# Performance work log

Measured on AMD Instinct MI355X. Metric: run time of the kernel, lower is better.

## Reference

```python
import jax, jax.numpy as jnp
import numpy as np

D_STATE = 8
DT_RANK = 8  # ceil(128/16)


def _grouped_1x1(x, w):
    # x: (B,H,W,Cin), w: (g, Cout//g, Cin//g)
    B, H, W, _ = x.shape
    g, o, i = w.shape
    xg = x.reshape(B, H, W, g, i)
    return jnp.einsum('bhwgi,goi->bhwgo', xg, w).reshape(B, H, W, g * o)


def setup_inputs() -> dict:
    key = jax.random.key(0)
    ks = jax.random.split(key, 16)
    B, H, W, C = 8, 64, 64, 128
    g = 4
    D = 128  # expand_dim = d_inner
    N = D_STATE
    R = DT_RANK
    inp = {}
    inp['x'] = jax.random.normal(ks[0], (B, H, W, C), dtype=jnp.float32)
    inp['w1'] = jax.random.normal(ks[1], (g, D // g, C // g), dtype=jnp.float32) * 0.1
    inp['dw'] = jax.random.normal(ks[2], (3, 3, 1, D), dtype=jnp.float32) * 0.1  # HWIO depthwise
    inp['in_proj_w'] = jax.random.normal(ks[3], (2 * D, D), dtype=jnp.float32) * 0.05
    inp['conv1d_w'] = jax.random.normal(ks[4], (D, 3), dtype=jnp.float32) * 0.1
    inp['conv1d_b'] = jax.random.normal(ks[5], (D,), dtype=jnp.float32) * 0.05
    inp['x_proj_w'] = jax.random.normal(ks[6], (R + 2 * N, D), dtype=jnp.float32) * 0.05
    inp['dt_proj_w'] = jax.random.normal(ks[7], (D, R), dtype=jnp.float32) * 0.05
    inp['dt_proj_b'] = jax.random.normal(ks[8], (D,), dtype=jnp.float32) * 0.05
    inp['A_log'] = jnp.log(jnp.tile(jnp.arange(1, N + 1, dtype=jnp.float32)[None, :], (D, 1)))
    inp['D_param'] = jnp.ones((D,), dtype=jnp.float32)
    inp['out_proj_w'] = jax.random.normal(ks[9], (D, D), dtype=jnp.float32) * 0.05
    inp['gamma'] = jnp.ones((D,), dtype=jnp.float32)
    inp['beta'] = jnp.zeros((D,), dtype=jnp.float32)
    inp['w2'] = jax.random.normal(ks[10], (g, D // g, C // g), dtype=jnp.float32) * 0.1
    inp['wout'] = jax.random.normal(ks[11], (g, C // g, D // g), dtype=jnp.float32) * 0.1
    return inp


def _mamba(x_seq, in_proj_w, conv1d_w, conv1d_b, x_proj_w, dt_proj_w, dt_proj_b, A_log, D_param, out_proj_w):
    # x_seq: (B, L, D)
    B, L, D = x_seq.shape
    N, R = D_STATE, DT_RANK
    xz = jnp.einsum('bld,ed->ble', x_seq, in_proj_w)  # (B,L,2D)
    u, z = xz[..., :D], xz[..., D:]
    # causal depthwise conv1d, kernel=3, left pad 2 (torch: padding=2, slice [:L])
    up = jnp.pad(u, ((0, 0), (2, 0), (0, 0)))
    u = (up[:, 0:L] * conv1d_w[:, 0] + up[:, 1:L + 1] * conv1d_w[:, 1]
         + up[:, 2:L + 2] * conv1d_w[:, 2] + conv1d_b)
    u = jax.nn.silu(u)
    x_dbl = jnp.einsum('bld,ed->ble', u, x_proj_w)  # (B,L,R+2N)
    dt = x_dbl[..., :R]
    Bm = x_dbl[..., R:R + N]
    Cm = x_dbl[..., R + N:]
    delta = jax.nn.softplus(jnp.einsum('blr,dr->bld', dt, dt_proj_w) + dt_proj_b)  # (B,L,D)
    A = -jnp.exp(A_log)  # (D,N)

    def step(h, inp):
        d_t, u_t, b_t, c_t = inp  # (B,D),(B,D),(B,N),(B,N)
        dA = jnp.exp(d_t[..., None] * A)            # (B,D,N)
        h = dA * h + (d_t * u_t)[..., None] * b_t[:, None, :]
        y_t = jnp.einsum('bdn,bn->bd', h, c_t)
        return h, y_t

    h0 = jnp.zeros((B, D, N), dtype=x_seq.dtype)
    xs = (jnp.swapaxes(delta, 0, 1), jnp.swapaxes(u, 0, 1),
          jnp.swapaxes(Bm, 0, 1), jnp.swapaxes(Cm, 0, 1))
    _, ys = jax.lax.scan(step, h0, xs)              # ys: (L,B,D)
    y = jnp.swapaxes(ys, 0, 1) + u * D_param
    y = y * jax.nn.silu(z)
    return jnp.einsum('bld,ed->ble', y, out_proj_w)


def reference(x, w1, dw, in_proj_w, conv1d_w, conv1d_b, x_proj_w, dt_proj_w, dt_proj_b,
              A_log, D_param, out_proj_w, gamma, beta, w2, wout):
    B, H, W, C = x.shape
    D = dw.shape[-1]
    x1 = _grouped_1x1(x, w1)  # (B,H,W,D)
    x1 = jax.lax.conv_general_dilated(
        x1, dw, window_strides=(1, 1), padding='SAME',
        feature_group_count=D, dimension_numbers=('NHWC', 'HWIO', 'NHWC'))
    x1 = jax.nn.silu(x1)
    x1_seq = x1.reshape(B, H * W, D)
    x1_seq = _mamba(x1_seq, in_proj_w, conv1d_w, conv1d_b, x_proj_w,
                    dt_proj_w, dt_proj_b, A_log, D_param, out_proj_w)
    x1 = x1_seq.reshape(B, H, W, D)
    mu = jnp.mean(x1, axis=-1, keepdims=True)
    var = jnp.mean(jnp.square(x1 - mu), axis=-1, keepdims=True)
    x1 = (x1 - mu) * jax.lax.rsqrt(var + 1e-5) * gamma + beta
    x2 = jax.nn.silu(_grouped_1x1(x, w2))
    x_fuse = x1 * x2
    return _grouped_1x1(x_fuse, wout)  # (B,H,W,C)
```

## Files before the change

kernel.cpp:

```cpp
#include <hip/hip_runtime.h>
#include <math.h>

#define B_    8
#define C_    128
#define D_    128
#define L_    4096
#define NPOS_ 32768
#define NC_   256
#define S_    16
#define MFL_  1048576

typedef __attribute__((ext_vector_type(8))) short short8;
typedef __attribute__((ext_vector_type(4))) float f32x4;

__device__ __forceinline__ float siluf(float x) { return x / (1.f + __expf(-x)); }
__device__ __forceinline__ float softplusf(float x) {
    if (x > 20.f) return x;
    return __logf(1.f + __expf(x));
}
__device__ __forceinline__ unsigned short f2bf(float f) {
    unsigned int u = __float_as_uint(f);
    u = (u + 0x7FFFu + ((u >> 16) & 1u)) >> 16;
    return (unsigned short)u;
}
__device__ __forceinline__ float bf2f(unsigned short h) {
    return __uint_as_float(((unsigned int)h) << 16);
}
__device__ __forceinline__ void scan_as(float dl, const float* Ar, bool fast, float* a) {
    if (fast) {
        float e1 = __expf(-dl);
        a[0] = e1;
        a[1] = e1 * e1;
        a[2] = a[1] * e1;
        a[3] = a[1] * a[1];
        a[4] = a[3] * e1;
        a[5] = a[3] * a[1];
        a[6] = a[5] * e1;
        a[7] = a[3] * a[3];
    } else {
        #pragma unroll
        for (int n = 0; n < 8; ++n) a[n] = __expf(dl * Ar[n]);
    }
}

__global__ __launch_bounds__(256) void k1_g1x1(const float* __restrict__ x,
                                               const float* __restrict__ w1,
                                               const float* __restrict__ w2,
                                               const float* __restrict__ inW,
                                               const float* __restrict__ OW,
                                               const float* __restrict__ xpw,
                                               unsigned short* __restrict__ inWb,
                                               unsigned short* __restrict__ OWb,
                                               unsigned short* __restrict__ xpwb,
                                               unsigned short* __restrict__ t1b,
                                               unsigned short* __restrict__ x2sb) {
    __shared__ float xs[16 * 128];
    int t = threadIdx.x;
    {
        int i = blockIdx.x * 51 + t;
        if (t < 51 && i < 52224) {
            if (i < 32768)      inWb[i] = f2bf(inW[i]);
            else if (i < 49152) OWb[i - 32768] = f2bf(OW[i - 32768]);
            else                xpwb[i - 49152] = f2bf(xpw[i - 49152]);
        }
    }
    int d = t & 127, ph = t >> 7;
    int g = d >> 5, o = d & 31;
    float w1r[32], w2r[32];
    #pragma unroll
    for (int i = 0; i < 32; ++i) {
        w1r[i] = w1[g * 1024 + o * 32 + i];
        w2r[i] = w2[g * 1024 + o * 32 + i];
    }
    int pos0 = blockIdx.x * 32;
    for (int it = 0; it < 2; ++it) {
        int p0 = pos0 + it * 16;
        #pragma unroll
        for (int q = 0; q < 2; ++q) {
            int fi = t * 2 + q;
            *(float4*)&xs[fi * 4] = *(const float4*)&x[p0 * 128 + fi * 4];
        }
        __syncthreads();
        #pragma unroll
        for (int q = 0; q < 8; ++q) {
            int pl = ph * 8 + q;
            float a1 = 0.f, a2 = 0.f;
            const float* xr = &xs[pl * 128 + g * 32];
            #pragma unroll
            for (int i4 = 0; i4 < 8; ++i4) {
                float4 xv = *(const float4*)&xr[i4 * 4];
                a1 += xv.x * w1r[i4*4] + xv.y * w1r[i4*4+1] + xv.z * w1r[i4*4+2] + xv.w * w1r[i4*4+3];
                a2 += xv.x * w2r[i4*4] + xv.y * w2r[i4*4+1] + xv.z * w2r[i4*4+2] + xv.w * w2r[i4*4+3];
            }
            int pos = p0 + pl;
            t1b[pos * 128 + d]  = f2bf(a1);
            x2sb[pos * 128 + d] = f2bf(siluf(a2));
        }
        __syncthreads();
    }
}

__global__ __launch_bounds__(128) void k2_dwconv(const unsigned short* __restrict__ t1b,
                                                 const float* __restrict__ dw,
                                                 unsigned short* __restrict__ x1cb) {
    int d = threadIdx.x;
    float dwr[9];
    #pragma unroll
    for (int k = 0; k < 9; ++k) dwr[k] = dw[k * 128 + d];
    int bid = blockIdx.x;
    int wt = bid & 15, ht = (bid >> 4) & 7, b = bid >> 7;
    int h0 = ht * 8, w0 = wt * 4;
    float rows[10][6];
    #pragma unroll
    for (int r = 0; r < 10; ++r) {
        int hh = h0 - 1 + r;
        bool hv = (hh >= 0) && (hh < 64);
        #pragma unroll
        for (int c = 0; c < 6; ++c) {
            int w = w0 - 1 + c;
            bool wvv = (w >= 0) && (w < 64);
            rows[r][c] = (hv && wvv) ? bf2f(t1b[((b * 64 + hh) * 64 + w) * 128 + d]) : 0.f;
        }
    }
    #pragma unroll
    for (int hi = 0; hi < 8; ++hi) {
        #pragma unroll
        for (int wi = 0; wi < 4; ++wi) {
            float acc = rows[hi][wi]     * dwr[0] + rows[hi][wi+1]   * dwr[1] + rows[hi][wi+2]   * dwr[2]
                      + rows[hi+1][wi]   * dwr[3] + rows[hi+1][wi+1] * dwr[4] + rows[hi+1][wi+2] * dwr[5]
                      + rows[hi+2][wi]   * dwr[6] + rows[hi+2][wi+1] * dwr[7] + rows[hi+2][wi+2] * dwr[8];
            x1cb[((b * 64 + h0 + hi) * 64 + w0 + wi) * 128 + d] = f2bf(siluf(acc));
        }
    }
}

__global__ __launch_bounds__(256) void k3_mfma(const unsigned short* __restrict__ Abf,
                                               const unsigned short* __restrict__ Bbf,
                                               unsigned short* __restrict__ urawb,
                                               unsigned short* __restrict__ zb) {
    __shared__ unsigned short Al[64 * 72];
    __shared__ unsigned short Bl[128 * 72];
    int t = threadIdx.x;
    int pos0 = (blockIdx.x >> 1) * 64;
    int half = blockIdx.x & 1;
    const unsigned short* Bh = Bbf + (size_t)half * 128 * 128;
    unsigned short* dst = half ? zb : urawb;
    int lane = t & 63, wv = t >> 6;
    int lanem = lane & 15, laneq = lane >> 4;
    f32x4 acc[8];
    #pragma unroll
    for (int i = 0; i < 8; ++i) acc[i] = (f32x4){0.f, 0.f, 0.f, 0.f};
    for (int kc = 0; kc < 2; ++kc) {
        #pragma unroll
        for (int q = 0; q < 2; ++q) {
            int c = t + q * 256;
            int row = c >> 3, col = c & 7;
            *(int4*)&Al[row * 72 + col * 8] = *(const int4*)&Abf[(pos0 + row) * 128 + kc * 64 + col * 8];
        }
        #pragma unroll
        for (int q = 0; q < 4; ++q) {
            int c = t + q * 256;
            int row = c >> 3, col = c & 7;
            *(int4*)&Bl[row * 72 + col * 8] = *(const int4*)&Bh[row * 128 + kc * 64 + col * 8];
        }
        __syncthreads();
        #pragma unroll
        for (int ks = 0; ks < 2; ++ks) {
            short8 af = *(const short8*)&Al[(wv * 16 + lanem) * 72 + ks * 32 + laneq * 8];
            #pragma unroll
            for (int ni = 0; ni < 8; ++ni) {
                short8 bfr = *(const short8*)&Bl[(ni * 16 + lanem) * 72 + ks * 32 + laneq * 8];
                acc[ni] = __builtin_amdgcn_mfma_f32_16x16x32_bf16(af, bfr, acc[ni], 0, 0, 0);
            }
        }
        __syncthreads();
    }
    #pragma unroll
    for (int ni = 0; ni < 8; ++ni)
        #pragma unroll
        for (int r = 0; r < 4; ++r) {
            int m = pos0 + wv * 16 + laneq * 4 + r;
            int n = ni * 16 + lanem;
            dst[m * 128 + n] = f2bf(acc[ni][r]);
        }
}

__global__ __launch_bounds__(256) void k45_convproj(const unsigned short* __restrict__ urawb,
                                                    const float* __restrict__ cw,
                                                    const float* __restrict__ cb,
                                                    const unsigned short* __restrict__ xpwb,
                                                    const float* __restrict__ dtw,
                                                    const float* __restrict__ dtb,
                                                    const float* __restrict__ A_log,
                                                    unsigned short* __restrict__ usb,
                                                    unsigned short* __restrict__ deltab,
                                                    float* __restrict__ Bm,
                                                    float* __restrict__ Cm,
                                                    float* __restrict__ cA,
                                                    float* __restrict__ cB) {
    __shared__ unsigned short uA[32 * 136];
    __shared__ unsigned short xB[32 * 136];
    __shared__ float xdb[32 * 36];
    int t = threadIdx.x;
    int d = t & 127, ph = t >> 7;
    for (int i = t; i < 32 * 128; i += 256) {
        int n = i >> 7, k = i & 127;
        xB[n * 136 + k] = (n < 24) ? xpwb[n * 128 + k] : (unsigned short)0;
    }
    float cw0 = cw[d * 3 + 0], cw1 = cw[d * 3 + 1], cw2 = cw[d * 3 + 2], cbr = cb[d];
    float dtwr[8];
    #pragma unroll
    for (int r = 0; r < 8; ++r) dtwr[r] = dtw[d * 8 + r];
    float dtbr = dtb[d];
    float Ar[8]; bool fast = true;
    #pragma unroll
    for (int n = 0; n < 8; ++n) {
        Ar[n] = -__expf(A_log[d * 8 + n]);
        fast = fast && (fabsf(Ar[n] + (float)(n + 1)) < 2e-3f);
    }

    int gpos0 = blockIdx.x * 32;
    int ll0 = (gpos0 & 4095) + ph * 16;
    int base = (gpos0 + ph * 16) * 128 + d;
    float ur0 = (ll0 >= 2) ? bf2f(urawb[base - 256]) : 0.f;
    float ur1 = (ll0 >= 1) ? bf2f(urawb[base - 128]) : 0.f;
    #pragma unroll
    for (int q = 0; q < 16; ++q) {
        float urq = bf2f(urawb[base + q * 128]);
        float v = siluf(ur0 * cw0 + ur1 * cw1 + urq * cw2 + cbr);
        unsigned short vb = f2bf(v);
        usb[base + q * 128] = vb;
        uA[(ph * 16 + q) * 136 + d] = vb;
        ur0 = ur1; ur1 = urq;
    }
    __syncthreads();
    int lane = t & 63, wv = t >> 6;
    int lanem = lane & 15, laneq = lane >> 4;
    int m0 = (wv & 1) * 16, n0 = (wv >> 1) * 16;
    f32x4 accx = (f32x4){0.f, 0.f, 0.f, 0.f};
    #pragma unroll
    for (int ks = 0; ks < 4; ++ks) {
        short8 af  = *(const short8*)&uA[(m0 + lanem) * 136 + ks * 32 + laneq * 8];
        short8 bfr = *(const short8*)&xB[(n0 + lanem) * 136 + ks * 32 + laneq * 8];
        accx = __builtin_amdgcn_mfma_f32_16x16x32_bf16(af, bfr, accx, 0, 0, 0);
    }
    #pragma unroll
    for (int r = 0; r < 4; ++r)
        xdb[(m0 + laneq * 4 + r) * 36 + n0 + lanem] = accx[r];
    __syncthreads();
    float h[8], ap[8];
    #pragma unroll
    for (int n = 0; n < 8; ++n) { h[n] = 0.f; ap[n] = 1.f; }
    #pragma unroll
    for (int q = 0; q < 16; ++q) {
        int pl = ph * 16 + q;
        float dt = dtbr;
        #pragma unroll
        for (int r = 0; r < 8; ++r) dt += xdb[pl * 36 + r] * dtwr[r];
        unsigned short dlb = f2bf(softplusf(dt));
        deltab[base + q * 128] = dlb;
        float dl = bf2f(dlb);
        float du = dl * bf2f(uA[pl * 136 + d]);
        float a[8];
        scan_as(dl, Ar, fast, a);
        #pragma unroll
        for (int n = 0; n < 8; ++n) {
            ap[n] *= a[n];
            h[n] = a[n] * h[n] + du * xdb[pl * 36 + 8 + n];
        }
    }
    int bH = gpos0 >> 12;
    int c  = ((gpos0 & 4095) >> 4) + ph;
    int obase = ((bH * NC_ + c) * 128 + d) * 8;
    *(float4*)&cA[obase]     = make_float4(ap[0], ap[1], ap[2], ap[3]);
    *(float4*)&cA[obase + 4] = make_float4(ap[4], ap[5], ap[6], ap[7]);
    *(float4*)&cB[obase]     = make_float4(h[0], h[1], h[2], h[3]);
    *(float4*)&cB[obase + 4] = make_float4(h[4], h[5], h[6], h[7]);
    for (int i = t; i < 512; i += 256) {
        int p = i >> 4, j = i & 15;
        float v = xdb[p * 36 + 8 + j];
        int gp = gpos0 + p;
        if (j < 8) Bm[gp * 8 + j] = v;
        else       Cm[gp * 8 + (j - 8)] = v;
    }
}

__global__ __launch_bounds__(128) void k6_scan2(const float* __restrict__ cA,
                                                const float* __restrict__ cB,
                                                float* __restrict__ carry) {
    int b = blockIdx.x >> 3;
    int slice = blockIdx.x & 7;
    int dn = slice * 128 + threadIdx.x;
    float h = 0.f;
    #pragma unroll 8
    for (int c = 0; c < NC_; ++c) {
        int idx = (b * NC_ + c) * 1024 + dn;
        float a  = cA[idx];
        float bv = cB[idx];
        carry[idx] = h;
        h = a * h + bv;
    }
}

__global__ __launch_bounds__(128) void k7_scan3(const unsigned short* __restrict__ deltab,
                                                const unsigned short* __restrict__ usb,
                                                const float* __restrict__ Bm,
                                                const float* __restrict__ Cm,
                                                const unsigned short* __restrict__ zb,
                                                const float* __restrict__ A_log,
                                                const float* __restrict__ Dp,
                                                const float* __restrict__ carry,
                                                unsigned short* __restrict__ ybf) {
    int d = threadIdx.x;
    int bc = blockIdx.x;
    int b = bc >> 8, c = bc & 255;
    float Ar[8]; bool fast = true;
    #pragma unroll
    for (int n = 0; n < 8; ++n) {
        Ar[n] = -__expf(A_log[d * 8 + n]);
        fast = fast && (fabsf(Ar[n] + (float)(n + 1)) < 2e-3f);
    }
    float Dpr = Dp[d];
    int cbase = ((b * NC_ + c) * 128 + d) * 8;
    float4 h0 = *(const float4*)&carry[cbase];
    float4 h1 = *(const float4*)&carry[cbase + 4];
    float h[8] = {h0.x, h0.y, h0.z, h0.w, h1.x, h1.y, h1.z, h1.w};
    int base  = (b * L_ + c * S_) * 128 + d;
    int bbase = (b * L_ + c * S_) * 8;
    #pragma unroll
    for (int s = 0; s < S_; ++s) {
        float dl = bf2f(deltab[base + s * 128]);
        float uv = bf2f(usb[base + s * 128]);
        float zv = bf2f(zb[base + s * 128]);
        float du = dl * uv;
        float4 bm0 = *(const float4*)&Bm[bbase + s * 8];
        float4 bm1 = *(const float4*)&Bm[bbase + s * 8 + 4];
        float4 cm0 = *(const float4*)&Cm[bbase + s * 8];
        float4 cm1 = *(const float4*)&Cm[bbase + s * 8 + 4];
        float a[8];
        scan_as(dl, Ar, fast, a);
        h[0] = a[0] * h[0] + du * bm0.x;
        h[1] = a[1] * h[1] + du * bm0.y;
        h[2] = a[2] * h[2] + du * bm0.z;
        h[3] = a[3] * h[3] + du * bm0.w;
        h[4] = a[4] * h[4] + du * bm1.x;
        h[5] = a[5] * h[5] + du * bm1.y;
        h[6] = a[6] * h[6] + du * bm1.z;
        h[7] = a[7] * h[7] + du * bm1.w;
        float yv = h[0] * cm0.x + h[1] * cm0.y + h[2] * cm0.z + h[3] * cm0.w
                 + h[4] * cm1.x + h[5] * cm1.y + h[6] * cm1.z + h[7] * cm1.w;
        yv = (yv + uv * Dpr) * siluf(zv);
        ybf[base + s * 128] = f2bf(yv);
    }
}

__global__ __launch_bounds__(256) void k8a_mfma(const unsigned short* __restrict__ Abf,
                                                const unsigned short* __restrict__ Bbf,
                                                unsigned short* __restrict__ xzb) {
    __shared__ unsigned short Al[64 * 72];
    __shared__ unsigned short Bl[128 * 72];
    int t = threadIdx.x;
    int pos0 = blockIdx.x * 64;
    int lane = t & 63, wv = t >> 6;
    int lanem = lane & 15, laneq = lane >> 4;
    f32x4 acc[8];
    #pragma unroll
    for (int i = 0; i < 8; ++i) acc[i] = (f32x4){0.f, 0.f, 0.f, 0.f};
    for (int kc = 0; kc < 2; ++kc) {
        #pragma unroll
        for (int q = 0; q < 2; ++q) {
            int c = t + q * 256;
            int row = c >> 3, col = c & 7;
            *(int4*)&Al[row * 72 + col * 8] = *(const int4*)&Abf[(pos0 + row) * 128 + kc * 64 + col * 8];
        }
        #pragma unroll
        for (int q = 0; q < 4; ++q) {
            int c = t + q * 256;
            int row = c >> 3, col = c & 7;
            *(int4*)&Bl[row * 72 + col * 8] = *(const int4*)&Bbf[row * 128 + kc * 64 + col * 8];
        }
        __syncthreads();
        #pragma unroll
        for (int ks = 0; ks < 2; ++ks) {
            short8 af = *(const short8*)&Al[(wv * 16 + lanem) * 72 + ks * 32 + laneq * 8];
            #pragma unroll
            for (int ni = 0; ni < 8; ++ni) {
                short8 bfr = *(const short8*)&Bl[(ni * 16 + lanem) * 72 + ks * 32 + laneq * 8];
                acc[ni] = __builtin_amdgcn_mfma_f32_16x16x32_bf16(af, bfr, acc[ni], 0, 0, 0);
            }
        }
        __syncthreads();
    }
    #pragma unroll
    for (int ni = 0; ni < 8; ++ni)
        #pragma unroll
        for (int r = 0; r < 4; ++r) {
            int m = pos0 + wv * 16 + laneq * 4 + r;
            int n = ni * 16 + lanem;
            xzb[m * 128 + n] = f2bf(acc[ni][r]);
        }
}

__global__ __launch_bounds__(256) void k8b_epi(const unsigned short* __restrict__ xzb,
                                               const float* __restrict__ gamma,
                                               const float* __restrict__ beta,
                                               const unsigned short* __restrict__ x2sb,
                                               const float* __restrict__ wout,
                                               float* __restrict__ out) {
    __shared__ float woutL[4 * 1160];
    __shared__ float gbL[256];
    int t = threadIdx.x;
    int pos0 = blockIdx.x * 64;
    for (int idx = t; idx < 4096; idx += 256) {
        int g = idx >> 10, r = idx & 1023, o = r >> 5, i = r & 31;
        woutL[g * 1160 + o * 36 + i] = wout[idx];
    }
    if (t < 128) gbL[t] = gamma[t];
    else         gbL[t] = beta[t - 128];
    __syncthreads();

    int g = t & 3, pos = t >> 2;
    int gpos = pos0 + pos;
    float v[32];
    #pragma unroll
    for (int i4 = 0; i4 < 8; ++i4) {
        ushort4 xv = *(const ushort4*)&xzb[gpos * 128 + g * 32 + i4 * 4];
        v[i4*4+0] = bf2f(xv.x); v[i4*4+1] = bf2f(xv.y);
        v[i4*4+2] = bf2f(xv.z); v[i4*4+3] = bf2f(xv.w);
    }
    float s = 0.f, s2 = 0.f;
    #pragma unroll
    for (int i = 0; i < 32; ++i) { s += v[i]; s2 += v[i] * v[i]; }
    s  += __shfl_xor(s, 1, 64);  s  += __shfl_xor(s, 2, 64);
    s2 += __shfl_xor(s2, 1, 64); s2 += __shfl_xor(s2, 2, 64);
    float m = s * (1.f / 128.f);
    float var = s2 * (1.f / 128.f) - m * m;
    float rstd = rsqrtf(var + 1e-5f);
    #pragma unroll
    for (int i4 = 0; i4 < 8; ++i4) {
        ushort4 xv = *(const ushort4*)&x2sb[gpos * 128 + g * 32 + i4 * 4];
        unsigned short xa[4] = {xv.x, xv.y, xv.z, xv.w};
        #pragma unroll
        for (int k = 0; k < 4; ++k) {
            int e = g * 32 + i4 * 4 + k;
            float vv = (v[i4 * 4 + k] - m) * rstd * gbL[e] + gbL[128 + e];
            v[i4 * 4 + k] = vv * bf2f(xa[k]);
        }
    }
    const float* wg = &woutL[g * 1160];
    int obase = gpos * 128 + g * 32;
    #pragma unroll
    for (int ob = 0; ob < 8; ++ob) {
        float o4[4];
        #pragma unroll
        for (int oo = 0; oo < 4; ++oo) {
            int o = ob * 4 + oo;
            float acc = 0.f;
            #pragma unroll
            for (int i4 = 0; i4 < 8; ++i4) {
                float4 wv4 = *(const float4*)&wg[o * 36 + i4 * 4];
                acc += v[i4*4] * wv4.x + v[i4*4+1] * wv4.y
                     + v[i4*4+2] * wv4.z + v[i4*4+3] * wv4.w;
            }
            o4[oo] = acc;
        }
        *(float4*)&out[obase + ob * 4] = make_float4(o4[0], o4[1], o4[2], o4[3]);
    }
}

extern "C" void kernel_launch(void* const* d_in, const int* in_sizes, int n_in,
                              void* d_out, int out_size, void* d_ws, size_t ws_size,
                              hipStream_t stream) {
    (void)in_sizes; (void)n_in; (void)out_size; (void)ws_size;
    const float* x         = (const float*)d_in[0];
    const float* w1        = (const float*)d_in[1];
    const float* dw        = (const float*)d_in[2];
    const float* in_proj_w = (const float*)d_in[3];
    const float* conv1d_w  = (const float*)d_in[4];
    const float* conv1d_b  = (const float*)d_in[5];
    const float* x_proj_w  = (const float*)d_in[6];
    const float* dt_proj_w = (const float*)d_in[7];
    const float* dt_proj_b = (const float*)d_in[8];
    const float* A_log     = (const float*)d_in[9];
    const float* D_param   = (const float*)d_in[10];
    const float* out_proj_w= (const float*)d_in[11];
    const float* gamma     = (const float*)d_in[12];
    const float* beta      = (const float*)d_in[13];
    const float* w2        = (const float*)d_in[14];
    const float* wout      = (const float*)d_in[15];
    float* out = (float*)d_out;

    float* ws = (float*)d_ws;
    unsigned short* x2sb   = (unsigned short*)(ws);
    unsigned short* t1b    = (unsigned short*)(ws + 2  * (size_t)MFL_);
    unsigned short* x1cb   = (unsigned short*)(ws + 4  * (size_t)MFL_);
    unsigned short* urawb  = (unsigned short*)(ws + 6  * (size_t)MFL_);
    unsigned short* zb     = (unsigned short*)(ws + 8  * (size_t)MFL_);
    unsigned short* ybf    = (unsigned short*)(ws + 10 * (size_t)MFL_);
    unsigned short* xzb    = (unsigned short*)(ws + 12 * (size_t)MFL_);
    unsigned short* usb    = (unsigned short*)(ws + 14 * (size_t)MFL_);
    unsigned short* deltab = (unsigned short*)(ws + 16 * (size_t)MFL_);
    float* Bm    = ws + 18 * (size_t)MFL_;
    float* Cm    = Bm + (size_t)NPOS_ * 8;
    float* cA    = Cm + (size_t)NPOS_ * 8;
    float* cB    = cA + 2 * (size_t)MFL_;
    float* carry = cB + 2 * (size_t)MFL_;
    unsigned short* inWb = (unsigned short*)(carry + 2 * (size_t)MFL_);
    unsigned short* OWb  = inWb + 32768;
    unsigned short* xpwb = OWb + 16384;

    k1_g1x1<<<1024, 256, 0, stream>>>(x, w1, w2, in_proj_w, out_proj_w, x_proj_w,
                                      inWb, OWb, xpwb, t1b, x2sb);
    k2_dwconv<<<1024, 128, 0, stream>>>(t1b, dw, x1cb);
    k3_mfma<<<1024, 256, 0, stream>>>(x1cb, inWb, urawb, zb);
    k45_convproj<<<1024, 256, 0, stream>>>(urawb, conv1d_w, conv1d_b, xpwb,
                                           dt_proj_w, dt_proj_b, A_log,
                                           usb, deltab, Bm, Cm, cA, cB);
    k6_scan2<<<64, 128, 0, stream>>>(cA, cB, carry);
    k7_scan3<<<2048, 128, 0, stream>>>(deltab, usb, Bm, Cm, zb, A_log, D_param, carry, ybf);
    k8a_mfma<<<512, 256, 0, stream>>>(ybf, OWb, xzb);
    k8b_epi<<<512, 256, 0, stream>>>(xzb, gamma, beta, x2sb, wout, out);
}
```

Baseline: 220.3 us.

## Fuse scan phase 3, out_proj MFMA and layernorm epilogue into one kernel

Merges the per-chunk scan output, the out_proj bf16 MFMA GEMM and the layernorm/gating/grouped-1x1 epilogue into a single kernel. Each 256-thread block handles 64 positions (4 chunks), writes y into shared memory as the GEMM A operand, then stages the GEMM result in shared memory as floats for the epilogue. This removes the global round trips for ybf and xzb and two kernel launches. In exchange the scan stage gets fewer blocks (512 instead of 2048), shared memory use per block rises, and there is less parallelism to hide the latency of the serial scan.

```diff
diff --git a/kernel.cpp b/kernel.cpp
--- a/kernel.cpp
+++ b/kernel.cpp
@@ -302,18 +302,36 @@
     }
 }
 
-__global__ __launch_bounds__(128) void k7_scan3(const unsigned short* __restrict__ deltab,
-                                                const unsigned short* __restrict__ usb,
-                                                const float* __restrict__ Bm,
-                                                const float* __restrict__ Cm,
-                                                const unsigned short* __restrict__ zb,
-                                                const float* __restrict__ A_log,
-                                                const float* __restrict__ Dp,
-                                                const float* __restrict__ carry,
-                                                unsigned short* __restrict__ ybf) {
-    int d = threadIdx.x;
-    int bc = blockIdx.x;
-    int b = bc >> 8, c = bc & 255;
+__global__ __launch_bounds__(256) void k7f_fused(const unsigned short* __restrict__ deltab,
+                                                 const unsigned short* __restrict__ usb,
+                                                 const float* __restrict__ Bm,
+                                                 const float* __restrict__ Cm,
+                                                 const unsigned short* __restrict__ zb,
+                                                 const float* __restrict__ A_log,
+                                                 const float* __restrict__ Dp,
+                                                 const float* __restrict__ carry,
+                                                 const unsigned short* __restrict__ OWb,
+                                                 const float* __restrict__ gamma,
+                                                 const float* __restrict__ beta,
+                                                 const unsigned short* __restrict__ x2sb,
+                                                 const float* __restrict__ wout,
+                                                 float* __restrict__ out) {
+    __shared__ __align__(16) char smem[37888];
+    unsigned short* yA = (unsigned short*)smem;
+    unsigned short* Bl = (unsigned short*)(smem + 18432);
+    float* xz = (float*)smem;
+    __shared__ float woutL[4 * 1160];
+    __shared__ float gbL[256];
+    int t = threadIdx.x;
+    for (int idx = t; idx < 4096; idx += 256) {
+        int g = idx >> 10, r = idx & 1023, o = r >> 5, i = r & 31;
+        woutL[g * 1160 + o * 36 + i] = wout[idx];
+    }
+    if (t < 128) gbL[t] = gamma[t];
+    else         gbL[t] = beta[t - 128];
+
+    int d = t & 127, ph = t >> 7;
+    int b = blockIdx.x >> 6, cblk = blockIdx.x & 63;
     float Ar[8]; bool fast = true;
     #pragma unroll
     for (int n = 0; n < 8; ++n) {
@@ -321,46 +339,44 @@
         fast = fast && (fabsf(Ar[n] + (float)(n + 1)) < 2e-3f);
     }
     float Dpr = Dp[d];
-    int cbase = ((b * NC_ + c) * 128 + d) * 8;
-    float4 h0 = *(const float4*)&carry[cbase];
-    float4 h1 = *(const float4*)&carry[cbase + 4];
-    float h[8] = {h0.x, h0.y, h0.z, h0.w, h1.x, h1.y, h1.z, h1.w};
-    int base  = (b * L_ + c * S_) * 128 + d;
-    int bbase = (b * L_ + c * S_) * 8;
-    #pragma unroll
-    for (int s = 0; s < S_; ++s) {
-        float dl = bf2f(deltab[base + s * 128]);
-        float uv = bf2f(usb[base + s * 128]);
-        float zv = bf2f(zb[base + s * 128]);
-        float du = dl * uv;
-        float4 bm0 = *(const float4*)&Bm[bbase + s * 8];
-        float4 bm1 = *(const float4*)&Bm[bbase + s * 8 + 4];
-        float4 cm0 = *(const float4*)&Cm[bbase + s * 8];
-        float4 cm1 = *(const float4*)&Cm[bbase + s * 8 + 4];
-        float a[8];
-        scan_as(dl, Ar, fast, a);
-        h[0] = a[0] * h[0] + du * bm0.x;
-        h[1] = a[1] * h[1] + du * bm0.y;
-        h[2] = a[2] * h[2] + du * bm0.z;
-        h[3] = a[3] * h[3] + du * bm0.w;
-        h[4] = a[4] * h[4] + du * bm1.x;
-        h[5] = a[5] * h[5] + du * bm1.y;
-        h[6] = a[6] * h[6] + du * bm1.z;
-        h[7] = a[7] * h[7] + du * bm1.w;
-        float yv = h[0] * cm0.x + h[1] * cm0.y + h[2] * cm0.z + h[3] * cm0.w
-                 + h[4] * cm1.x + h[5] * cm1.y + h[6] * cm1.z + h[7] * cm1.w;
-        yv = (yv + uv * Dpr) * siluf(zv);
-        ybf[base + s * 128] = f2bf(yv);
-    }
-}
-
-__global__ __launch_bounds__(256) void k8a_mfma(const unsigned short* __restrict__ Abf,
-                                                const unsigned short* __restrict__ Bbf,
-                                                unsigned short* __restrict__ xzb) {
-    __shared__ unsigned short Al[64 * 72];
-    __shared__ unsigned short Bl[128 * 72];
-    int t = threadIdx.x;
-    int pos0 = blockIdx.x * 64;
+    int ybase = (d >> 6) * (64 * 72) + (d & 63);
+    for (int cc = 0; cc < 2; ++cc) {
+        int cl = ph * 2 + cc;
+        int c = cblk * 4 + cl;
+        int cbase = ((b * NC_ + c) * 128 + d) * 8;
+        float4 h0 = *(const float4*)&carry[cbase];
+        float4 h1 = *(const float4*)&carry[cbase + 4];
+        float h[8] = {h0.x, h0.y, h0.z, h0.w, h1.x, h1.y, h1.z, h1.w};
+        int base  = (b * L_ + c * S_) * 128 + d;
+        int bbase = (b * L_ + c * S_) * 8;
+        #pragma unroll
+        for (int s = 0; s < S_; ++s) {
+            float dl = bf2f(deltab[base + s * 128]);
+            float uv = bf2f(usb[base + s * 128]);
+            float zv = bf2f(zb[base + s * 128]);
+            float du = dl * uv;
+            float4 bm0 = *(const float4*)&Bm[bbase + s * 8];
+            float4 bm1 = *(const float4*)&Bm[bbase + s * 8 + 4];
+            float4 cm0 = *(const float4*)&Cm[bbase + s * 8];
+            float4 cm1 = *(const float4*)&Cm[bbase + s * 8 + 4];
+            float a[8];
+            scan_as(dl, Ar, fast, a);
+            h[0] = a[0] * h[0] + du * bm0.x;
+            h[1] = a[1] * h[1] + du * bm0.y;
+            h[2] = a[2] * h[2] + du * bm0.z;
+            h[3] = a[3] * h[3] + du * bm0.w;
+            h[4] = a[4] * h[4] + du * bm1.x;
+            h[5] = a[5] * h[5] + du * bm1.y;
+            h[6] = a[6] * h[6] + du * bm1.z;
+            h[7] = a[7] * h[7] + du * bm1.w;
+            float yv = h[0] * cm0.x + h[1] * cm0.y + h[2] * cm0.z + h[3] * cm0.w
+                     + h[4] * cm1.x + h[5] * cm1.y + h[6] * cm1.z + h[7] * cm1.w;
+            yv = (yv + uv * Dpr) * siluf(zv);
+            yA[ybase + (cl * 16 + s) * 72] = f2bf(yv);
+        }
+    }
+    __syncthreads();
+
     int lane = t & 63, wv = t >> 6;
     int lanem = lane & 15, laneq = lane >> 4;
     f32x4 acc[8];
@@ -368,21 +384,15 @@
     for (int i = 0; i < 8; ++i) acc[i] = (f32x4){0.f, 0.f, 0.f, 0.f};
     for (int kc = 0; kc < 2; ++kc) {
         #pragma unroll
-        for (int q = 0; q < 2; ++q) {
-            int c = t + q * 256;
-            int row = c >> 3, col = c & 7;
-            *(int4*)&Al[row * 72 + col * 8] = *(const int4*)&Abf[(pos0 + row) * 128 + kc * 64 + col * 8];
-        }
-        #pragma unroll
         for (int q = 0; q < 4; ++q) {
-            int c = t + q * 256;
-            int row = c >> 3, col = c & 7;
-            *(int4*)&Bl[row * 72 + col * 8] = *(const int4*)&Bbf[row * 128 + kc * 64 + col * 8];
+            int cidx = t + q * 256;
+            int row = cidx >> 3, col = cidx & 7;
+            *(int4*)&Bl[row * 72 + col * 8] = *(const int4*)&OWb[row * 128 + kc * 64 + col * 8];
         }
         __syncthreads();
         #pragma unroll
         for (int ks = 0; ks < 2; ++ks) {
-            short8 af = *(const short8*)&Al[(wv * 16 + lanem) * 72 + ks * 32 + laneq * 8];
+            short8 af = *(const short8*)&yA[kc * (64 * 72) + (wv * 16 + lanem) * 72 + ks * 32 + laneq * 8];
             #pragma unroll
             for (int ni = 0; ni < 8; ++ni) {
                 short8 bfr = *(const short8*)&Bl[(ni * 16 + lanem) * 72 + ks * 32 + laneq * 8];
@@ -392,41 +402,24 @@
         __syncthreads();
     }
     #pragma unroll
-    for (int ni = 0; ni < 8; ++ni)
-        #pragma unroll
-        for (int r = 0; r < 4; ++r) {
-            int m = pos0 + wv * 16 + laneq * 4 + r;
-            int n = ni * 16 + lanem;
-            xzb[m * 128 + n] = f2bf(acc[ni][r]);
-        }
-}
-
-__global__ __launch_bounds__(256) void k8b_epi(const unsigned short* __restrict__ xzb,
-                                               const float* __restrict__ gamma,
-                                               const float* __restrict__ beta,
-                                               const unsigned short* __restrict__ x2sb,
-                                               const float* __restrict__ wout,
-                                               float* __restrict__ out) {
-    __shared__ float woutL[4 * 1160];
-    __shared__ float gbL[256];
-    int t = threadIdx.x;
-    int pos0 = blockIdx.x * 64;
-    for (int idx = t; idx < 4096; idx += 256) {
-        int g = idx >> 10, r = idx & 1023, o = r >> 5, i = r & 31;
-        woutL[g * 1160 + o * 36 + i] = wout[idx];
-    }
-    if (t < 128) gbL[t] = gamma[t];
-    else         gbL[t] = beta[t - 128];
+    for (int ni = 0; ni < 8; ++ni) {
+        int ch = ni * 16 + lanem;
+        int col = ch + ((ch >> 5) << 2);
+        #pragma unroll
+        for (int r = 0; r < 4; ++r)
+            xz[(wv * 16 + laneq * 4 + r) * 148 + col] = bf2f(f2bf(acc[ni][r]));
+    }
     __syncthreads();
 
     int g = t & 3, pos = t >> 2;
-    int gpos = pos0 + pos;
+    int gpos = b * L_ + cblk * 64 + pos;
+    const float* xrow0 = &xz[pos * 148 + g * 36];
     float v[32];
     #pragma unroll
     for (int i4 = 0; i4 < 8; ++i4) {
-        ushort4 xv = *(const ushort4*)&xzb[gpos * 128 + g * 32 + i4 * 4];
-        v[i4*4+0] = bf2f(xv.x); v[i4*4+1] = bf2f(xv.y);
-        v[i4*4+2] = bf2f(xv.z); v[i4*4+3] = bf2f(xv.w);
+        float4 xv = *(const float4*)&xrow0[i4 * 4];
+        v[i4*4+0] = xv.x; v[i4*4+1] = xv.y;
+        v[i4*4+2] = xv.z; v[i4*4+3] = xv.w;
     }
     float s = 0.f, s2 = 0.f;
     #pragma unroll
@@ -447,6 +440,7 @@
             v[i4 * 4 + k] = vv * bf2f(xa[k]);
         }
     }
+
     const float* wg = &woutL[g * 1160];
     int obase = gpos * 128 + g * 32;
     #pragma unroll
@@ -455,14 +449,14 @@
         #pragma unroll
         for (int oo = 0; oo < 4; ++oo) {
             int o = ob * 4 + oo;
-            float acc = 0.f;
+            float acc2 = 0.f;
             #pragma unroll
             for (int i4 = 0; i4 < 8; ++i4) {
                 float4 wv4 = *(const float4*)&wg[o * 36 + i4 * 4];
-                acc += v[i4*4] * wv4.x + v[i4*4+1] * wv4.y
-                     + v[i4*4+2] * wv4.z + v[i4*4+3] * wv4.w;
+                acc2 += v[i4*4] * wv4.x + v[i4*4+1] * wv4.y
+                      + v[i4*4+2] * wv4.z + v[i4*4+3] * wv4.w;
             }
-            o4[oo] = acc;
+            o4[oo] = acc2;
         }
         *(float4*)&out[obase + ob * 4] = make_float4(o4[0], o4[1], o4[2], o4[3]);
     }
@@ -496,8 +490,6 @@
     unsigned short* x1cb   = (unsigned short*)(ws + 4  * (size_t)MFL_);
     unsigned short* urawb  = (unsigned short*)(ws + 6  * (size_t)MFL_);
     unsigned short* zb     = (unsigned short*)(ws + 8  * (size_t)MFL_);
-    unsigned short* ybf    = (unsigned short*)(ws + 10 * (size_t)MFL_);
-    unsigned short* xzb    = (unsigned short*)(ws + 12 * (size_t)MFL_);
     unsigned short* usb    = (unsigned short*)(ws + 14 * (size_t)MFL_);
     unsigned short* deltab = (unsigned short*)(ws + 16 * (size_t)MFL_);
     float* Bm    = ws + 18 * (size_t)MFL_;
@@ -517,7 +509,6 @@
                                            dt_proj_w, dt_proj_b, A_log,
                                            usb, deltab, Bm, Cm, cA, cB);
     k6_scan2<<<64, 128, 0, stream>>>(cA, cB, carry);
-    k7_scan3<<<2048, 128, 0, stream>>>(deltab, usb, Bm, Cm, zb, A_log, D_param, carry, ybf);
-    k8a_mfma<<<512, 256, 0, stream>>>(ybf, OWb, xzb);
-    k8b_epi<<<512, 256, 0, stream>>>(xzb, gamma, beta, x2sb, wout, out);
-}
+    k7f_fused<<<512, 256, 0, stream>>>(deltab, usb, Bm, Cm, zb, A_log, D_param,
+                                       carry, OWb, gamma, beta, x2sb, wout, out);
+}
```

New measurement: 212.9 us. -3.4%, faster.
